# Optimization experiments

Measured on AMD Instinct MI355X. Metric: run time of the kernel, lower is better.

## Reference

```python
import jax, jax.numpy as jnp
import numpy as np

M, P, B, TLEN = 512, 256, 128, 1024

def setup_inputs() -> dict:
    key = jax.random.key(0)
    k1, k2, k3, k4, k5, k6 = jax.random.split(key, 6)
    d_t = jax.random.normal(k1, (1, B, P), dtype=jnp.float32)
    s_t = jax.random.normal(k2, (1, B, P), dtype=jnp.float32)
    H = jax.random.normal(k3, (B, TLEN, M), dtype=jnp.float32)
    # torch.nn.Linear weights: shape [out_features, in_features]
    W_d = jax.random.normal(k4, (M, 2 * P), dtype=jnp.float32) / np.sqrt(2 * P)
    U_d = jax.random.normal(k5, (M, M), dtype=jnp.float32) / np.sqrt(M)
    v_d = jax.random.normal(k6, (1, M), dtype=jnp.float32) / np.sqrt(M)
    return {"d_t": d_t, "s_t": s_t, "H": H, "T": TLEN, "W_d": W_d, "U_d": U_d, "v_d": v_d}

def reference(d_t, s_t, H, T, W_d, U_d, v_d):
    # query: cat([d_t, s_t], dim=2) -> [1, B, 2p]; permute(1,0,2) -> [B, 1, 2p]
    query = jnp.concatenate([d_t, s_t], axis=2).transpose(1, 0, 2)  # [B, 1, 2p]
    # W_d(query) broadcast over T instead of materializing the repeat (same math)
    wq = jnp.einsum('boc,mc->bom', query, W_d)          # [B, 1, m]
    uh = jnp.einsum('btm,nm->btn', H, U_d)              # [B, T, m]
    beta = jnp.tanh(wq + uh)                            # [B, T, m]
    score = jnp.einsum('btm,om->bto', beta, v_d)        # [B, T, 1]
    score = score.transpose(0, 2, 1)                    # [B, 1, T]
    return jax.nn.softmax(score, axis=2)
```

## Files before the change

### kernel.cpp

```cpp
#include <hip/hip_runtime.h>
#include <hip/hip_bf16.h>
#include <stdint.h>

#define NB   128
#define NT   1024
#define NM   512
#define NP   256

typedef __attribute__((ext_vector_type(8))) short bf16x8;
typedef __attribute__((ext_vector_type(4))) float f32x4;

__device__ __forceinline__ unsigned short f2bf(float f) {
    union { float f; uint32_t u; } x; x.f = f;
    uint32_t u = x.u + 0x7FFFu + ((x.u >> 16) & 1u);
    return (unsigned short)(u >> 16);
}

__global__ void cvt_u_kernel(const float* __restrict__ U, unsigned short* __restrict__ Ub) {
    int idx = blockIdx.x * blockDim.x + threadIdx.x;
    float4 u = reinterpret_cast<const float4*>(U)[idx];
    ushort4 o;
    o.x = f2bf(u.x); o.y = f2bf(u.y); o.z = f2bf(u.z); o.w = f2bf(u.w);
    reinterpret_cast<ushort4*>(Ub)[idx] = o;
}

__global__ void wq_kernel(const float* __restrict__ d_t, const float* __restrict__ s_t,
                          const float* __restrict__ W, float* __restrict__ wq) {
    int g = blockIdx.x * blockDim.x + threadIdx.x;
    int b = g >> 9;
    int n = g & 511;
    const float* Wn = W + (size_t)n * 512;
    const float* dt = d_t + (size_t)b * NP;
    const float* st = s_t + (size_t)b * NP;
    float s = 0.f;
    #pragma unroll 4
    for (int c = 0; c < NP; c += 4) {
        float4 w0 = *reinterpret_cast<const float4*>(Wn + c);
        float4 q0 = *reinterpret_cast<const float4*>(dt + c);
        s += w0.x * q0.x + w0.y * q0.y + w0.z * q0.z + w0.w * q0.w;
        float4 w1 = *reinterpret_cast<const float4*>(Wn + NP + c);
        float4 q1 = *reinterpret_cast<const float4*>(st + c);
        s += w1.x * q1.x + w1.y * q1.y + w1.z * q1.z + w1.w * q1.w;
    }
    wq[g] = s;
}

__global__ __launch_bounds__(256, 2)
void score_kernel(const float* __restrict__ H, const unsigned short* __restrict__ Ub,
                  const float* __restrict__ wq, const float* __restrict__ v_d,
                  float* __restrict__ out) {
    __shared__ unsigned short As[64 * 40];
    __shared__ unsigned short Bs[512 * 40];
    __shared__ float s_score[64];

    const int tid  = threadIdx.x;
    const int b    = blockIdx.y;
    const int t0   = blockIdx.x * 64;
    const int lane = tid & 63;
    const int w    = tid >> 6;
    const int lr   = lane & 15;
    const int lq   = lane >> 4;

    const float* Hb = H + ((size_t)b * NT + t0) * NM;

    f32x4 acc[4][8];
    #pragma unroll
    for (int i = 0; i < 4; ++i)
        #pragma unroll
        for (int j = 0; j < 8; ++j)
            acc[i][j] = (f32x4){0.f, 0.f, 0.f, 0.f};

    for (int kk = 0; kk < 16; ++kk) {
        const int m0 = kk * 32;
        #pragma unroll
        for (int i = 0; i < 2; ++i) {
            int idx = tid + i * 256;
            int r   = idx >> 3;
            int c4  = (idx & 7) * 4;
            float4 v = *reinterpret_cast<const float4*>(Hb + (size_t)r * NM + m0 + c4);
            ushort4 o;
            o.x = f2bf(v.x); o.y = f2bf(v.y); o.z = f2bf(v.z); o.w = f2bf(v.w);
            *reinterpret_cast<ushort4*>(&As[r * 40 + c4]) = o;
        }
        #pragma unroll
        for (int i = 0; i < 8; ++i) {
            int idx = tid + i * 256;
            int r   = idx >> 2;
            int c8  = (idx & 3) * 8;
            int4 vv = *reinterpret_cast<const int4*>(Ub + (size_t)r * NM + m0 + c8);
            *reinterpret_cast<int4*>(&Bs[r * 40 + c8]) = vv;
        }
        __syncthreads();

        bf16x8 a[4], bq[8];
        #pragma unroll
        for (int i = 0; i < 4; ++i)
            a[i] = *reinterpret_cast<const bf16x8*>(&As[(i * 16 + lr) * 40 + lq * 8]);
        #pragma unroll
        for (int j = 0; j < 8; ++j)
            bq[j] = *reinterpret_cast<const bf16x8*>(&Bs[(w * 128 + j * 16 + lr) * 40 + lq * 8]);
        #pragma unroll
        for (int i = 0; i < 4; ++i)
            #pragma unroll
            for (int j = 0; j < 8; ++j)
                acc[i][j] = __builtin_amdgcn_mfma_f32_16x16x32_bf16(a[i], bq[j], acc[i][j], 0, 0, 0);
        __syncthreads();
    }

    if (tid < 64) s_score[tid] = 0.f;
    __syncthreads();

    const float* wqb = wq + (size_t)b * NM;
    float vv[8], wv[8];
    #pragma unroll
    for (int j = 0; j < 8; ++j) {
        int n = w * 128 + j * 16 + lr;
        vv[j] = v_d[n];
        wv[j] = wqb[n];
    }
    #pragma unroll
    for (int i = 0; i < 4; ++i) {
        #pragma unroll
        for (int r = 0; r < 4; ++r) {
            float s = 0.f;
            #pragma unroll
            for (int j = 0; j < 8; ++j)
                s += vv[j] * tanhf(wv[j] + acc[i][j][r]);
            #pragma unroll
            for (int off = 1; off < 16; off <<= 1)
                s += __shfl_xor(s, off, 64);
            if (lr == 0) atomicAdd(&s_score[i * 16 + lq * 4 + r], s);
        }
    }
    __syncthreads();
    if (tid < 64) out[(size_t)b * NT + t0 + tid] = s_score[tid];
}

__global__ void softmax_kernel(float* __restrict__ out) {
    const int b   = blockIdx.x;
    const int tid = threadIdx.x;
    float* p = out + (size_t)b * NT;
    float4 v = reinterpret_cast<float4*>(p)[tid];
    float m = fmaxf(fmaxf(v.x, v.y), fmaxf(v.z, v.w));
    #pragma unroll
    for (int off = 32; off >= 1; off >>= 1)
        m = fmaxf(m, __shfl_xor(m, off, 64));
    __shared__ float red[8];
    const int wv = tid >> 6;
    if ((tid & 63) == 0) red[wv] = m;
    __syncthreads();
    m = fmaxf(fmaxf(red[0], red[1]), fmaxf(red[2], red[3]));
    float e0 = __expf(v.x - m), e1 = __expf(v.y - m);
    float e2 = __expf(v.z - m), e3 = __expf(v.w - m);
    float s = e0 + e1 + e2 + e3;
    #pragma unroll
    for (int off = 32; off >= 1; off >>= 1)
        s += __shfl_xor(s, off, 64);
    if ((tid & 63) == 0) red[4 + wv] = s;
    __syncthreads();
    s = red[4] + red[5] + red[6] + red[7];
    float inv = 1.f / s;
    float4 o;
    o.x = e0 * inv; o.y = e1 * inv; o.z = e2 * inv; o.w = e3 * inv;
    reinterpret_cast<float4*>(p)[tid] = o;
}

extern "C" void kernel_launch(void* const* d_in, const int* in_sizes, int n_in,
                              void* d_out, int out_size, void* d_ws, size_t ws_size,
                              hipStream_t stream) {
    const float* d_t = (const float*)d_in[0];
    const float* s_t = (const float*)d_in[1];
    const float* H   = (const float*)d_in[2];
    const float* W_d = (const float*)d_in[4];
    const float* U_d = (const float*)d_in[5];
    const float* v_d = (const float*)d_in[6];
    float* out = (float*)d_out;

    unsigned short* Ub = (unsigned short*)d_ws;
    float* wq = (float*)((char*)d_ws + 512 * 1024);

    cvt_u_kernel<<<256, 256, 0, stream>>>(U_d, Ub);
    wq_kernel<<<256, 256, 0, stream>>>(d_t, s_t, W_d, wq);
    score_kernel<<<dim3(NT / 64, NB), 256, 0, stream>>>(H, Ub, wq, v_d, out);
    softmax_kernel<<<NB, 256, 0, stream>>>(out);
}
```

Baseline: 496.0 us.

## Load MFMA operands directly from global memory, drop LDS staging, use fast tanh

The score kernel stops staging H and U tiles through shared memory with two barriers per K step. Each lane now loads its MFMA operand fragments straight from global memory, converting H to bf16 in registers with a perm-based round-half-up pack, and the K loop is unrolled by two. tanhf is replaced by an exp/rcp approximation. This removes the LDS traffic and synchronisation, but every wave now fetches H rows redundantly (the four waves read the same A data) and uses strided, less coalesced global loads. The bf16 rounding and the tanh approximation also change numerics slightly.

```diff
diff --git a/kernel.cpp b/kernel.cpp
--- a/kernel.cpp
+++ b/kernel.cpp
@@ -10,18 +10,32 @@
 typedef __attribute__((ext_vector_type(8))) short bf16x8;
 typedef __attribute__((ext_vector_type(4))) float f32x4;
 
-__device__ __forceinline__ unsigned short f2bf(float f) {
-    union { float f; uint32_t u; } x; x.f = f;
-    uint32_t u = x.u + 0x7FFFu + ((x.u >> 16) & 1u);
-    return (unsigned short)(u >> 16);
+__device__ __forceinline__ uint32_t bfpair(float a, float b) {
+    uint32_t ua = __float_as_uint(a) + 0x8000u;
+    uint32_t ub = __float_as_uint(b) + 0x8000u;
+    return __builtin_amdgcn_perm(ub, ua, 0x07060302u);
+}
+
+__device__ __forceinline__ bf16x8 pack8(float4 f0, float4 f1) {
+    union { bf16x8 v; uint32_t u[4]; } r;
+    r.u[0] = bfpair(f0.x, f0.y);
+    r.u[1] = bfpair(f0.z, f0.w);
+    r.u[2] = bfpair(f1.x, f1.y);
+    r.u[3] = bfpair(f1.z, f1.w);
+    return r.v;
+}
+
+__device__ __forceinline__ float fast_tanh(float x) {
+    float e = __expf(2.0f * x);
+    return 1.0f - 2.0f * __builtin_amdgcn_rcpf(e + 1.0f);
 }
 
 __global__ void cvt_u_kernel(const float* __restrict__ U, unsigned short* __restrict__ Ub) {
     int idx = blockIdx.x * blockDim.x + threadIdx.x;
     float4 u = reinterpret_cast<const float4*>(U)[idx];
-    ushort4 o;
-    o.x = f2bf(u.x); o.y = f2bf(u.y); o.z = f2bf(u.z); o.w = f2bf(u.w);
-    reinterpret_cast<ushort4*>(Ub)[idx] = o;
+    uint32_t lo = bfpair(u.x, u.y);
+    uint32_t hi = bfpair(u.z, u.w);
+    reinterpret_cast<uint2*>(Ub)[idx] = make_uint2(lo, hi);
 }
 
 __global__ void wq_kernel(const float* __restrict__ d_t, const float* __restrict__ s_t,
@@ -49,8 +63,6 @@
 void score_kernel(const float* __restrict__ H, const unsigned short* __restrict__ Ub,
                   const float* __restrict__ wq, const float* __restrict__ v_d,
                   float* __restrict__ out) {
-    __shared__ unsigned short As[64 * 40];
-    __shared__ unsigned short Bs[512 * 40];
     __shared__ float s_score[64];
 
     const int tid  = threadIdx.x;
@@ -61,7 +73,8 @@
     const int lr   = lane & 15;
     const int lq   = lane >> 4;
 
-    const float* Hb = H + ((size_t)b * NT + t0) * NM;
+    const float* pA = H + ((size_t)b * NT + t0 + lr) * NM + lq * 8;
+    const unsigned short* pB = Ub + ((size_t)(w * 128 + lr)) * NM + lq * 8;
 
     f32x4 acc[4][8];
     #pragma unroll
@@ -70,41 +83,29 @@
         for (int j = 0; j < 8; ++j)
             acc[i][j] = (f32x4){0.f, 0.f, 0.f, 0.f};
 
+    #pragma unroll 2
     for (int kk = 0; kk < 16; ++kk) {
-        const int m0 = kk * 32;
+        const int k0 = kk * 32;
+
+        bf16x8 a[4];
         #pragma unroll
-        for (int i = 0; i < 2; ++i) {
-            int idx = tid + i * 256;
-            int r   = idx >> 3;
-            int c4  = (idx & 7) * 4;
-            float4 v = *reinterpret_cast<const float4*>(Hb + (size_t)r * NM + m0 + c4);
-            ushort4 o;
-            o.x = f2bf(v.x); o.y = f2bf(v.y); o.z = f2bf(v.z); o.w = f2bf(v.w);
-            *reinterpret_cast<ushort4*>(&As[r * 40 + c4]) = o;
+        for (int i = 0; i < 4; ++i) {
+            const float* ap = pA + (size_t)i * 16 * NM + k0;
+            float4 f0 = *reinterpret_cast<const float4*>(ap);
+            float4 f1 = *reinterpret_cast<const float4*>(ap + 4);
+            a[i] = pack8(f0, f1);
         }
-        #pragma unroll
-        for (int i = 0; i < 8; ++i) {
-            int idx = tid + i * 256;
-            int r   = idx >> 2;
-            int c8  = (idx & 3) * 8;
-            int4 vv = *reinterpret_cast<const int4*>(Ub + (size_t)r * NM + m0 + c8);
-            *reinterpret_cast<int4*>(&Bs[r * 40 + c8]) = vv;
-        }
-        __syncthreads();
 
-        bf16x8 a[4], bq[8];
-        #pragma unroll
-        for (int i = 0; i < 4; ++i)
-            a[i] = *reinterpret_cast<const bf16x8*>(&As[(i * 16 + lr) * 40 + lq * 8]);
+        bf16x8 bq[8];
         #pragma unroll
         for (int j = 0; j < 8; ++j)
-            bq[j] = *reinterpret_cast<const bf16x8*>(&Bs[(w * 128 + j * 16 + lr) * 40 + lq * 8]);
+            bq[j] = *reinterpret_cast<const bf16x8*>(pB + (size_t)j * 16 * NM + k0);
+
         #pragma unroll
         for (int i = 0; i < 4; ++i)
             #pragma unroll
             for (int j = 0; j < 8; ++j)
                 acc[i][j] = __builtin_amdgcn_mfma_f32_16x16x32_bf16(a[i], bq[j], acc[i][j], 0, 0, 0);
-        __syncthreads();
     }
 
     if (tid < 64) s_score[tid] = 0.f;
@@ -125,7 +126,7 @@
             float s = 0.f;
             #pragma unroll
             for (int j = 0; j < 8; ++j)
-                s += vv[j] * tanhf(wv[j] + acc[i][j][r]);
+                s += vv[j] * fast_tanh(wv[j] + acc[i][j][r]);
             #pragma unroll
             for (int off = 1; off < 16; off <<= 1)
                 s += __shfl_xor(s, off, 64);
```

Result: slower. 587.2 us (+18.4%).
